# Kernel optimization log

Measured on AMD Instinct MI355X. Metric: run time of the kernel, lower is better.

## Reference

```python
import jax, jax.numpy as jnp
import numpy as np


def setup_inputs() -> dict:
    key = jax.random.key(0)
    x = jax.random.normal(key, (16, 256, 4096), dtype=jnp.float32)  # (B, C, N)
    return {"x": x}


def reference(x):
    # Original: sigmoid(avgpool_lastdim(x^T @ x)) == sigmoid(x^T @ mean(x, -1))
    # x: (B, C, N). m: (B, C). scores: (B, N).
    m = jnp.mean(x, axis=-1)
    scores = jnp.einsum('bcn,bc->bn', x, m)
    out = jax.nn.sigmoid(scores)
    return out[:, None, None, :]  # (B, 1, 1, N)
```

## Files before the change

### kernel.cpp

```cpp
#include <hip/hip_runtime.h>


#define B_DIM 16
#define C_DIM 256
#define N_DIM 4096

__global__ __launch_bounds__(256) void mean_rows_kernel(
    const float* __restrict__ x, float* __restrict__ m) {
  const int row = blockIdx.x;
  const float4* xr =
      reinterpret_cast<const float4*>(x + (size_t)row * N_DIM);
  float s = 0.0f;
#pragma unroll
  for (int i = 0; i < 4; ++i) {
    float4 v = xr[threadIdx.x + i * 256];
    s += (v.x + v.y) + (v.z + v.w);
  }
#pragma unroll
  for (int off = 32; off > 0; off >>= 1) s += __shfl_down(s, off, 64);
  __shared__ float wsum[4];
  const int lane = threadIdx.x & 63;
  const int wid = threadIdx.x >> 6;
  if (lane == 0) wsum[wid] = s;
  __syncthreads();
  if (threadIdx.x == 0) {
    float t = (wsum[0] + wsum[1]) + (wsum[2] + wsum[3]);
    m[row] = t * (1.0f / (float)N_DIM);
  }
}

__global__ __launch_bounds__(256) void score_kernel(
    const float* __restrict__ x, const float* __restrict__ m,
    float* __restrict__ out) {
  const int nblocks_per_b = N_DIM / 256;
  const int b = blockIdx.x / nblocks_per_b;
  const int nblk = blockIdx.x % nblocks_per_b;
  const int n = nblk * 256 + threadIdx.x;

  __shared__ float ms[C_DIM];
  ms[threadIdx.x] = m[b * C_DIM + threadIdx.x];
  __syncthreads();

  const float* xb = x + (size_t)b * C_DIM * N_DIM + n;
  float s = 0.0f;
#pragma unroll 8
  for (int c = 0; c < C_DIM; ++c) {
    s += xb[(size_t)c * N_DIM] * ms[c];
  }
  out[(size_t)b * N_DIM + n] = 1.0f / (1.0f + expf(-s));
}

extern "C" void kernel_launch(void* const* d_in, const int* in_sizes, int n_in,
                              void* d_out, int out_size, void* d_ws,
                              size_t ws_size, hipStream_t stream) {
  const float* x = (const float*)d_in[0];
  float* out = (float*)d_out;
  float* m = (float*)d_ws;

  mean_rows_kernel<<<B_DIM * C_DIM, 256, 0, stream>>>(x, m);
  score_kernel<<<B_DIM * (N_DIM / 256), 256, 0, stream>>>(x, m, out);
}
```

Before: 102.4 us.

## Split channel reduction across blocks with partial sums and separate sigmoid reduce

The score kernel is replaced by a split-C kernel. Each block handles 16 channels for a 1024-wide N tile using float4 loads, and writes partial sums to workspace. A third kernel then sums the 16 partials and applies a fast-exp sigmoid. The goal is more blocks and memory-level parallelism than the original 256-block launch, whose threads walked 256 serial strided loads. The cost is an extra launch and an extra 4 MB partial write and read.

```diff
diff --git a/kernel.cpp b/kernel.cpp
--- a/kernel.cpp
+++ b/kernel.cpp
@@ -4,12 +4,14 @@
 #define B_DIM 16
 #define C_DIM 256
 #define N_DIM 4096
+#define CSPLIT 16
+#define CCHUNK (C_DIM / CSPLIT)
+#define NTILE 1024
 
 __global__ __launch_bounds__(256) void mean_rows_kernel(
     const float* __restrict__ x, float* __restrict__ m) {
   const int row = blockIdx.x;
-  const float4* xr =
-      reinterpret_cast<const float4*>(x + (size_t)row * N_DIM);
+  const float4* xr = reinterpret_cast<const float4*>(x + (size_t)row * N_DIM);
   float s = 0.0f;
 #pragma unroll
   for (int i = 0; i < 4; ++i) {
@@ -29,25 +31,53 @@
   }
 }
 
-__global__ __launch_bounds__(256) void score_kernel(
+__global__ __launch_bounds__(256) void partial_score_kernel(
     const float* __restrict__ x, const float* __restrict__ m,
-    float* __restrict__ out) {
-  const int nblocks_per_b = N_DIM / 256;
-  const int b = blockIdx.x / nblocks_per_b;
-  const int nblk = blockIdx.x % nblocks_per_b;
-  const int n = nblk * 256 + threadIdx.x;
+    float* __restrict__ partials) {
+  const int bid = blockIdx.x;
+  const int cs = bid & (CSPLIT - 1);
+  const int nt = (bid >> 4) & 3;
+  const int b = bid >> 6;
 
-  __shared__ float ms[C_DIM];
-  ms[threadIdx.x] = m[b * C_DIM + threadIdx.x];
+  __shared__ float ms[CCHUNK];
+  if (threadIdx.x < CCHUNK)
+    ms[threadIdx.x] = m[b * C_DIM + cs * CCHUNK + threadIdx.x];
   __syncthreads();
 
-  const float* xb = x + (size_t)b * C_DIM * N_DIM + n;
-  float s = 0.0f;
-#pragma unroll 8
-  for (int c = 0; c < C_DIM; ++c) {
-    s += xb[(size_t)c * N_DIM] * ms[c];
+  const int n0 = nt * NTILE + threadIdx.x * 4;
+  const float* xb =
+      x + (size_t)b * C_DIM * N_DIM + (size_t)(cs * CCHUNK) * N_DIM + n0;
+
+  float4 acc = make_float4(0.f, 0.f, 0.f, 0.f);
+#pragma unroll
+  for (int c = 0; c < CCHUNK; ++c) {
+    float4 v = *reinterpret_cast<const float4*>(xb + (size_t)c * N_DIM);
+    float w = ms[c];
+    acc.x += v.x * w;
+    acc.y += v.y * w;
+    acc.z += v.z * w;
+    acc.w += v.w * w;
   }
-  out[(size_t)b * N_DIM + n] = 1.0f / (1.0f + expf(-s));
+  float* p = partials + ((size_t)cs * B_DIM + b) * N_DIM + n0;
+  *reinterpret_cast<float4*>(p) = acc;
+}
+
+__global__ __launch_bounds__(256) void reduce_sigmoid_kernel(
+    const float* __restrict__ partials, float* __restrict__ out) {
+  const int i4 = (blockIdx.x * 256 + threadIdx.x) * 4;
+  float4 s = make_float4(0.f, 0.f, 0.f, 0.f);
+#pragma unroll
+  for (int cs = 0; cs < CSPLIT; ++cs) {
+    float4 v = *reinterpret_cast<const float4*>(
+        partials + (size_t)cs * (B_DIM * N_DIM) + i4);
+    s.x += v.x; s.y += v.y; s.z += v.z; s.w += v.w;
+  }
+  float4 o;
+  o.x = 1.0f / (1.0f + __expf(-s.x));
+  o.y = 1.0f / (1.0f + __expf(-s.y));
+  o.z = 1.0f / (1.0f + __expf(-s.z));
+  o.w = 1.0f / (1.0f + __expf(-s.w));
+  *reinterpret_cast<float4*>(out + i4) = o;
 }
 
 extern "C" void kernel_launch(void* const* d_in, const int* in_sizes, int n_in,
@@ -56,7 +86,11 @@
   const float* x = (const float*)d_in[0];
   float* out = (float*)d_out;
   float* m = (float*)d_ws;
+  float* partials = (float*)d_ws + 4096;
 
   mean_rows_kernel<<<B_DIM * C_DIM, 256, 0, stream>>>(x, m);
-  score_kernel<<<B_DIM * (N_DIM / 256), 256, 0, stream>>>(x, m, out);
+  partial_score_kernel<<<B_DIM * (N_DIM / NTILE) * CSPLIT, 256, 0, stream>>>(
+      x, m, partials);
+  reduce_sigmoid_kernel<<<(B_DIM * N_DIM) / 1024, 256, 0, stream>>>(partials,
+                                                                    out);
 }
```

New measurement: 99.91 us. 2.4% less time.
